# Kernel optimization log

Measured on AMD Instinct MI355X. Metric: run time of the kernel, lower is better.

The kernel has to match this reference:

```python
import jax, jax.numpy as jnp
import numpy as np

NUM_HEADS = 4
WINDOW = 3

def setup_inputs() -> dict:
    key = jax.random.key(0)
    ks = jax.random.split(key, 6)
    B, V, C, H, W = 4, 6, 256, 32, 32
    s = 0.02
    return {
        "x": jax.random.normal(ks[0], (B, V, C, H, W), jnp.float32),
        "Wq": jax.random.normal(ks[1], (C, C), jnp.float32) * s,
        "bq": jnp.zeros((C,), jnp.float32),
        "Wk": jax.random.normal(ks[2], (V * C, C), jnp.float32) * s,
        "bk": jnp.zeros((C,), jnp.float32),
        "Wv": jax.random.normal(ks[3], (V * C, C), jnp.float32) * s,
        "bv": jnp.zeros((C,), jnp.float32),
        "Wo": jax.random.normal(ks[4], (C, C), jnp.float32) * s,
        "bo": jnp.zeros((C,), jnp.float32),
    }

def reference(x, Wq, bq, Wk, bk, Wv, bv, Wo, bo):
    B, V, C, H, W = x.shape
    HW = H * W
    S = HW * V  # query sequence length
    nh = NUM_HEADS
    hd = C // nh
    # q: [B, V, H, W, C] -> [B, S, C]
    q_in = jnp.transpose(x, (0, 1, 3, 4, 2)).reshape(B, S, C)
    # k/v input: [B, H, W, V, C] -> [B, HW, V*C]
    kv_in = jnp.transpose(x, (0, 3, 4, 1, 2)).reshape(B, HW, V * C)
    q = q_in @ Wq + bq
    k = kv_in @ Wk + bk
    v = kv_in @ Wv + bv
    q = q.reshape(B, S, nh, hd).transpose(0, 2, 1, 3)    # [B, nh, S, hd]
    k = k.reshape(B, HW, nh, hd).transpose(0, 2, 1, 3)   # [B, nh, HW, hd]
    v = v.reshape(B, HW, nh, hd).transpose(0, 2, 1, 3)   # [B, nh, HW, hd]
    logits = jnp.einsum("bhqd,bhkd->bhqk", q, k) / jnp.sqrt(jnp.float32(hd))
    # Faithful mask: row i has ones in columns [max(0,i-W), i+W] (clipped to HW cols);
    # it is ADDED as mask * -1e9, masking OUT the diagonal window (as in source).
    i = jnp.arange(S)[:, None]
    j = jnp.arange(HW)[None, :]
    mask = ((j >= i - WINDOW) & (j < i + WINDOW + 1)).astype(logits.dtype)
    logits = logits + mask * (-1e9)
    attn = jax.nn.softmax(logits, axis=-1)
    out = jnp.einsum("bhqk,bhkd->bhqd", attn, v)         # [B, nh, S, hd]
    out = out.transpose(0, 2, 1, 3).reshape(B, S, C)
    out = out @ Wo + bo
    return x.reshape(B * V, C, H, W) + out.reshape(B * V, C, H, W)
```

## Files before the change

### kernel.cpp

```cpp
#include <hip/hip_runtime.h>
#include <cstddef>

namespace {

constexpr int B=4, V=6, C=256, HWS=1024, S=6144, NH=4, HD=64, VC=1536;

typedef short short8  __attribute__((ext_vector_type(8)));
typedef short short4v __attribute__((ext_vector_type(4)));
typedef float f32x4   __attribute__((ext_vector_type(4)));

__device__ inline short f2bf(float f){
  union{float f; unsigned u;} v; v.f=f;
  unsigned r = v.u + 0x7fffu + ((v.u>>16)&1u);
  return (short)(r>>16);
}

__device__ inline void tr_tile(const float* in, int inRow, short* out, int outRow,
                               int r0, int c0, short* T , int t){
  {
    const int rr=t>>2, cc=(t&3)*16;
    const float* p = in + (size_t)(r0+rr)*inRow + c0 + cc;
    short tmp[16];
    #pragma unroll
    for(int j=0;j<4;j++){
      const float4 f=*(const float4*)(p+j*4);
      tmp[j*4+0]=f2bf(f.x); tmp[j*4+1]=f2bf(f.y);
      tmp[j*4+2]=f2bf(f.z); tmp[j*4+3]=f2bf(f.w);
    }
    *(short8*)&T[rr*72+cc]   = *(short8*)&tmp[0];
    *(short8*)&T[rr*72+cc+8] = *(short8*)&tmp[8];
  }
  __syncthreads();
  {
    const int cc=t>>2, rr0=(t&3)*16;
    short tmp[16];
    #pragma unroll
    for(int j=0;j<16;j++) tmp[j]=T[(rr0+j)*72+cc];
    short* o = out + (size_t)(c0+cc)*outRow + r0 + rr0;
    *(short8*)o     = *(short8*)&tmp[0];
    *(short8*)(o+8) = *(short8*)&tmp[8];
  }
}

__global__ __launch_bounds__(256) void prep_x(const float* __restrict__ x, short* __restrict__ xb){
  __shared__ short T[64*72];
  const int bv=blockIdx.z;
  tr_tile(x + (size_t)bv*C*HWS, HWS, xb + (size_t)bv*HWS*C, C,
          blockIdx.y*64, blockIdx.x*64, T, threadIdx.x);
}

__global__ __launch_bounds__(256) void prep_w(const float* Wq,const float* Wk,const float* Wv,const float* Wo,
                                              short* WqT, short* WkT, short* WvT, short* WoT){
  __shared__ short T[64*72];
  const int z=blockIdx.y;
  const float* in; short* out; int R;
  if(z==0){in=Wq; out=WqT; R=C;}
  else if(z==1){in=Wo; out=WoT; R=C;}
  else if(z==2){in=Wk; out=WkT; R=VC;}
  else         {in=Wv; out=WvT; R=VC;}
  const int tilesC=C/64, ntiles=(R/64)*tilesC;
  const int tile=blockIdx.x;
  if(tile>=ntiles) return;
  tr_tile(in, C, out, R, (tile/tilesC)*64, (tile%tilesC)*64, T, threadIdx.x);
}

template<int MODE>
__global__ __launch_bounds__(256) void qo_gemm(const short* __restrict__ A, const short* __restrict__ BT,
                                               const float* __restrict__ bias, const float* __restrict__ xres,
                                               void* __restrict__ outv){
  __shared__ __align__(16) short As[128*72];
  __shared__ __align__(16) short Bs[64*72];
  const int n0=blockIdx.x*64, r0=blockIdx.y*128;
  const int t=threadIdx.x, lane=t&63, w=t>>6, quad=lane>>4, ln=lane&15;

  f32x4 acc[2][4];
  #pragma unroll
  for(int rt=0;rt<2;rt++)
    #pragma unroll
    for(int nt=0;nt<4;nt++) acc[rt][nt]=(f32x4)0.f;

  for(int k0=0;k0<C;k0+=64){
    if(k0) __syncthreads();
    { const int r=t>>1, c=(t&1)*32;
      const short* p = A + (size_t)(r0+r)*C + k0 + c;
      #pragma unroll
      for(int j=0;j<4;j++) *(short8*)&As[r*72+c+j*8] = *(const short8*)(p+j*8);
    }
    { const int n=t>>2, c=(t&3)*16;
      const short* p = BT + (size_t)(n0+n)*C + k0 + c;
      *(short8*)&Bs[n*72+c]   = *(const short8*)p;
      *(short8*)&Bs[n*72+c+8] = *(const short8*)(p+8);
    }
    __syncthreads();
    #pragma unroll
    for(int s=0;s<2;s++){
      short8 af0=*(short8*)&As[(w*32+ln)*72    + s*32+quad*8];
      short8 af1=*(short8*)&As[(w*32+16+ln)*72 + s*32+quad*8];
      #pragma unroll
      for(int nt=0;nt<4;nt++){
        const short8 bf=*(short8*)&Bs[(nt*16+ln)*72 + s*32+quad*8];
        acc[0][nt]=__builtin_amdgcn_mfma_f32_16x16x32_bf16(af0,bf,acc[0][nt],0,0,0);
        acc[1][nt]=__builtin_amdgcn_mfma_f32_16x16x32_bf16(af1,bf,acc[1][nt],0,0,0);
      }
    }
  }

  constexpr float QSCALE = 0.18033688011112042f;
  float bcol[4];
  #pragma unroll
  for(int nt=0;nt<4;nt++) bcol[nt]=bias[n0+nt*16+ln];
  #pragma unroll
  for(int rt=0;rt<2;rt++)
    #pragma unroll
    for(int nt=0;nt<4;nt++)
      #pragma unroll
      for(int i=0;i<4;i++){
        const int row=r0+w*32+rt*16+quad*4+i, col=n0+nt*16+ln;
        const float vv=acc[rt][nt][i]+bcol[nt];
        if constexpr(MODE==0) ((short*)outv)[(size_t)row*C+col]=f2bf(vv*QSCALE);
        else ((float*)outv)[(size_t)row*C+col]=vv + xres[(size_t)row*C+col];
      }
}

__global__ __launch_bounds__(256) void kv_gemm(const short* __restrict__ xb,
                                               const short* __restrict__ WkT, const short* __restrict__ WvT,
                                               const float* __restrict__ bk, const float* __restrict__ bv,
                                               short* __restrict__ Kpack, short* __restrict__ Vpack){
  __shared__ __align__(16) short As[64*72], Bk[64*72], Bv[64*72];
  const int n0=blockIdx.x*64, r0=blockIdx.y*64;
  const int b=r0>>10, hw0=r0&1023;
  const int h=n0>>6, bh=b*NH+h;
  const int t=threadIdx.x, lane=t&63, w=t>>6, quad=lane>>4, ln=lane&15;

  f32x4 ak[4], av[4];
  #pragma unroll
  for(int nt=0;nt<4;nt++){ ak[nt]=(f32x4)0.f; av[nt]=(f32x4)0.f; }

  const int sr=t>>2, sc=(t&3)*16;
  for(int k0=0;k0<VC;k0+=64){
    if(k0) __syncthreads();
    const int v=k0>>8, c0=k0&255;
    { const short* p = xb + (size_t)((b*V+v)*HWS + hw0+sr)*C + c0 + sc;
      *(short8*)&As[sr*72+sc]   = *(const short8*)p;
      *(short8*)&As[sr*72+sc+8] = *(const short8*)(p+8); }
    { const short* p = WkT + (size_t)(n0+sr)*VC + k0 + sc;
      *(short8*)&Bk[sr*72+sc]   = *(const short8*)p;
      *(short8*)&Bk[sr*72+sc+8] = *(const short8*)(p+8); }
    { const short* p = WvT + (size_t)(n0+sr)*VC + k0 + sc;
      *(short8*)&Bv[sr*72+sc]   = *(const short8*)p;
      *(short8*)&Bv[sr*72+sc+8] = *(const short8*)(p+8); }
    __syncthreads();
    #pragma unroll
    for(int s=0;s<2;s++){
      const short8 af=*(short8*)&As[(w*16+ln)*72 + s*32+quad*8];
      #pragma unroll
      for(int nt=0;nt<4;nt++){
        const short8 kf=*(short8*)&Bk[(nt*16+ln)*72 + s*32+quad*8];
        const short8 vf=*(short8*)&Bv[(nt*16+ln)*72 + s*32+quad*8];
        ak[nt]=__builtin_amdgcn_mfma_f32_16x16x32_bf16(af,kf,ak[nt],0,0,0);
        av[nt]=__builtin_amdgcn_mfma_f32_16x16x32_bf16(af,vf,av[nt],0,0,0);
      }
    }
  }

  float bkc[4], bvc[4];
  #pragma unroll
  for(int nt=0;nt<4;nt++){ bkc[nt]=bk[n0+nt*16+ln]; bvc[nt]=bv[n0+nt*16+ln]; }

  {
    short* vq = Vpack + ((size_t)(bh*64 + (hw0>>4) + w))*1024;
    #pragma unroll
    for(int nt=0;nt<4;nt++){
      short4v vp;
      #pragma unroll
      for(int i=0;i<4;i++) vp[i]=f2bf(av[nt][i]+bvc[nt]);
      *(short4v*)(vq + nt*256 + lane*4) = vp;
    }
  }

  __syncthreads();
  #pragma unroll
  for(int nt=0;nt<4;nt++)
    #pragma unroll
    for(int i=0;i<4;i++)
      As[(w*16+quad*4+i)*72 + nt*16+ln] = f2bf(ak[nt][i]+bkc[nt]);
  __syncthreads();
  {
    short* kp = Kpack + ((size_t)(bh*64 + (hw0>>4) + w))*1024;
    #pragma unroll
    for(int half=0; half<2; half++){
      const short8 f = *(short8*)&As[(w*16+ln)*72 + half*32 + quad*8];
      *(short8*)(kp + half*512 + lane*8) = f;
    }
  }
}

__global__ __launch_bounds__(256) void attn_k(const short* __restrict__ q, const short* __restrict__ Kpack,
                                              const short* __restrict__ Vpack, short* __restrict__ ao){
  __shared__ float obuf[64*68];
  __shared__ float lbuf[4][64];
  const int blk=blockIdx.x;
  const int bh=(blk&7)*2 + ((blk>>3)&1);
  const int qt=blk>>4;
  const int b=bh>>2, h=bh&3;
  const int s0=qt*64;
  const int t=threadIdx.x, lane=t&63, w=t>>6, quad=lane>>4, ln=lane&15;

  short8 qf[4][2];
  #pragma unroll
  for(int nt=0;nt<4;nt++)
    #pragma unroll
    for(int s=0;s<2;s++)
      qf[nt][s]=*(const short8*)&q[(size_t)(b*S+s0+nt*16+ln)*C + h*HD + s*32+quad*8];

  f32x4 o[4][4];
  #pragma unroll
  for(int dt=0;dt<4;dt++)
    #pragma unroll
    for(int nt=0;nt<4;nt++) o[dt][nt]=(f32x4)0.f;
  float l[4]={0.f,0.f,0.f,0.f};

  const short* kp = Kpack + ((size_t)(bh*64 + w))*1024;
  const short* vp = Vpack + ((size_t)(bh*64 + w))*1024;

  short8  kf0=*(const short8*)(kp + lane*8);
  short8  kf1=*(const short8*)(kp + 512 + lane*8);
  short4v vf[4];
  #pragma unroll
  for(int dt=0;dt<4;dt++) vf[dt]=*(const short4v*)(vp + dt*256 + lane*4);

  #pragma unroll 1
  for(int j0=0;j0<HWS;j0+=64){
    const size_t adv = (j0+64<HWS) ? 4096 : 0;
    kp += adv; vp += adv;
    const short8  nkf0=*(const short8*)(kp + lane*8);
    const short8  nkf1=*(const short8*)(kp + 512 + lane*8);
    short4v nvf[4];
    #pragma unroll
    for(int dt=0;dt<4;dt++) nvf[dt]=*(const short4v*)(vp + dt*256 + lane*4);

    f32x4 sa[4];
    #pragma unroll
    for(int nt=0;nt<4;nt++) sa[nt]=(f32x4)0.f;
    #pragma unroll
    for(int nt=0;nt<4;nt++){
      sa[nt]=__builtin_amdgcn_mfma_f32_16x16x32_bf16(kf0,qf[nt][0],sa[nt],0,0,0);
      sa[nt]=__builtin_amdgcn_mfma_f32_16x16x32_bf16(kf1,qf[nt][1],sa[nt],0,0,0);
    }

    const int kmin=j0+w*16;
    if(kmin+15 >= s0-3 && kmin <= s0+66){
      #pragma unroll
      for(int nt=0;nt<4;nt++){
        const int ig=s0+nt*16+ln;
        #pragma unroll
        for(int i=0;i<4;i++){
          const int jg=kmin+quad*4+i;
          if((unsigned)(jg-ig+3)<=6u) sa[nt][i]=-100.f;
        }
      }
    }

    short4v pt[4];
    #pragma unroll
    for(int nt=0;nt<4;nt++){
      #pragma unroll
      for(int i=0;i<4;i++){
        const float p=__builtin_amdgcn_exp2f(sa[nt][i]);
        l[nt]+=p;
        union{float f;unsigned u;} pu; pu.f=p;
        pt[nt][i]=(short)(pu.u>>16);
      }
    }

    #pragma unroll
    for(int dt=0;dt<4;dt++)
      #pragma unroll
      for(int nt=0;nt<4;nt++)
        o[dt][nt]=__builtin_amdgcn_mfma_f32_16x16x16bf16_1k(vf[dt],pt[nt],o[dt][nt],0,0,0);

    kf0=nkf0; kf1=nkf1;
    #pragma unroll
    for(int dt=0;dt<4;dt++) vf[dt]=nvf[dt];
  }

  #pragma unroll
  for(int nt=0;nt<4;nt++){
    l[nt]+=__shfl_xor(l[nt],16);
    l[nt]+=__shfl_xor(l[nt],32);
  }
  if(quad==0){
    #pragma unroll
    for(int nt=0;nt<4;nt++) lbuf[w][nt*16+ln]=l[nt];
  }
  for(int r=0;r<4;r++){
    if(w==r){
      #pragma unroll
      for(int dt=0;dt<4;dt++)
        #pragma unroll
        for(int nt=0;nt<4;nt++)
          #pragma unroll
          for(int i=0;i<4;i++){
            const int idx=(dt*16+quad*4+i)*68 + nt*16+ln;
            if(r==0) obuf[idx]=o[dt][nt][i]; else obuf[idx]+=o[dt][nt][i];
          }
    }
    __syncthreads();
  }

  {
    const int row=t>>2, dg=t&3;
    const float linv=1.0f/(lbuf[0][row]+lbuf[1][row]+lbuf[2][row]+lbuf[3][row]);
    short tmp[16];
    #pragma unroll
    for(int j=0;j<16;j++) tmp[j]=f2bf(obuf[(dg*16+j)*68+row]*linv);
    short* op = ao + (size_t)(b*S+s0+row)*C + h*HD + dg*16;
    *(short8*)op     = *(short8*)&tmp[0];
    *(short8*)(op+8) = *(short8*)&tmp[8];
  }
}

}

extern "C" void kernel_launch(void* const* d_in, const int* in_sizes, int n_in,
                              void* d_out, int out_size, void* d_ws, size_t ws_size,
                              hipStream_t stream) {
  const float* x  = (const float*)d_in[0];
  const float* Wq = (const float*)d_in[1];
  const float* bq = (const float*)d_in[2];
  const float* Wk = (const float*)d_in[3];
  const float* bk = (const float*)d_in[4];
  const float* Wv = (const float*)d_in[5];
  const float* bv = (const float*)d_in[6];
  const float* Wo = (const float*)d_in[7];
  const float* bo = (const float*)d_in[8];
  float* out = (float*)d_out;

  char* p = (char*)d_ws;
  const size_t szBS=(size_t)B*S*C*2, szK=(size_t)B*HWS*C*2;
  short* xb   =(short*)p; p+=szBS;
  short* qb   =(short*)p; p+=szBS;
  short* aob  =(short*)p; p+=szBS;
  short* Kpack=(short*)p; p+=szK;
  short* Vpack=(short*)p; p+=szK;
  short* WqT=(short*)p; p+=(size_t)C*C*2;
  short* WoT=(short*)p; p+=(size_t)C*C*2;
  short* WkT=(short*)p; p+=(size_t)C*VC*2;
  short* WvT=(short*)p; p+=(size_t)C*VC*2;

  prep_x<<<dim3(16,4,B*V), 256, 0, stream>>>(x, xb);
  prep_w<<<dim3(96,4),     256, 0, stream>>>(Wq,Wk,Wv,Wo, WqT,WkT,WvT,WoT);
  qo_gemm<0><<<dim3(4, (B*S)/128), 256, 0, stream>>>(xb, WqT, bq, nullptr, qb);
  kv_gemm<<<dim3(4, (B*HWS)/64),  256, 0, stream>>>(xb, WkT, WvT, bk, bv, Kpack, Vpack);
  attn_k<<<dim3(B*NH*(S/64)),     256, 0, stream>>>(qb, Kpack, Vpack, aob);
  qo_gemm<1><<<dim3(4, (B*S)/128), 256, 0, stream>>>(aob, WoT, bo, x, out);
}
```

Baseline: 203.6 us.

## Merge prep and projection launches, restructure attention K/V prefetch

Result: faster. 196.3 us (-3.6%).

```diff
diff --git a/kernel.cpp b/kernel.cpp
--- a/kernel.cpp
+++ b/kernel.cpp
@@ -14,6 +14,9 @@
   unsigned r = v.u + 0x7fffu + ((v.u>>16)&1u);
   return (short)(r>>16);
 }
+__device__ inline unsigned fbits(float f){
+  union{float f; unsigned u;} v; v.f=f; return v.u;
+}
 
 __device__ inline void tr_tile(const float* in, int inRow, short* out, int outRow,
                                int r0, int c0, short* T , int t){
@@ -42,37 +45,36 @@
   }
 }
 
-__global__ __launch_bounds__(256) void prep_x(const float* __restrict__ x, short* __restrict__ xb){
+__global__ __launch_bounds__(256) void prep(const float* __restrict__ x,
+                                            const float* __restrict__ Wq, const float* __restrict__ Wk,
+                                            const float* __restrict__ Wv, const float* __restrict__ Wo,
+                                            short* __restrict__ xb, short* __restrict__ WqT,
+                                            short* __restrict__ WkT, short* __restrict__ WvT,
+                                            short* __restrict__ WoT){
   __shared__ short T[64*72];
-  const int bv=blockIdx.z;
-  tr_tile(x + (size_t)bv*C*HWS, HWS, xb + (size_t)bv*HWS*C, C,
-          blockIdx.y*64, blockIdx.x*64, T, threadIdx.x);
-}
-
-__global__ __launch_bounds__(256) void prep_w(const float* Wq,const float* Wk,const float* Wv,const float* Wo,
-                                              short* WqT, short* WkT, short* WvT, short* WoT){
-  __shared__ short T[64*72];
-  const int z=blockIdx.y;
-  const float* in; short* out; int R;
-  if(z==0){in=Wq; out=WqT; R=C;}
-  else if(z==1){in=Wo; out=WoT; R=C;}
-  else if(z==2){in=Wk; out=WkT; R=VC;}
-  else         {in=Wv; out=WvT; R=VC;}
-  const int tilesC=C/64, ntiles=(R/64)*tilesC;
-  const int tile=blockIdx.x;
-  if(tile>=ntiles) return;
-  tr_tile(in, C, out, R, (tile/tilesC)*64, (tile%tilesC)*64, T, threadIdx.x);
+  const int blk=blockIdx.x;
+  if(blk<1536){
+    const int bx=blk&15, by=(blk>>4)&3, bv=blk>>6;
+    tr_tile(x + (size_t)bv*C*HWS, HWS, xb + (size_t)bv*HWS*C, C, by*64, bx*64, T, threadIdx.x);
+  } else {
+    const int idx=blk-1536;
+    const int tile=idx%96, z=idx/96;
+    const float* in; short* out; int R;
+    if(z==0){in=Wq; out=WqT; R=C;}
+    else if(z==1){in=Wo; out=WoT; R=C;}
+    else if(z==2){in=Wk; out=WkT; R=VC;}
+    else         {in=Wv; out=WvT; R=VC;}
+    const int tilesC=C/64, ntiles=(R/64)*tilesC;
+    if(tile>=ntiles) return;
+    tr_tile(in, C, out, R, (tile/tilesC)*64, (tile%tilesC)*64, T, threadIdx.x);
+  }
 }
 
 template<int MODE>
-__global__ __launch_bounds__(256) void qo_gemm(const short* __restrict__ A, const short* __restrict__ BT,
-                                               const float* __restrict__ bias, const float* __restrict__ xres,
-                                               void* __restrict__ outv){
-  __shared__ __align__(16) short As[128*72];
-  __shared__ __align__(16) short Bs[64*72];
-  const int n0=blockIdx.x*64, r0=blockIdx.y*128;
+__device__ inline void qo_body(const short* __restrict__ A, const short* __restrict__ BT,
+                               const float* __restrict__ bias, const float* __restrict__ xres,
+                               void* __restrict__ outv, short* As, short* Bs, int n0, int r0){
   const int t=threadIdx.x, lane=t&63, w=t>>6, quad=lane>>4, ln=lane&15;
-
   f32x4 acc[2][4];
   #pragma unroll
   for(int rt=0;rt<2;rt++)
@@ -122,15 +124,27 @@
       }
 }
 
-__global__ __launch_bounds__(256) void kv_gemm(const short* __restrict__ xb,
-                                               const short* __restrict__ WkT, const short* __restrict__ WvT,
-                                               const float* __restrict__ bk, const float* __restrict__ bv,
-                                               short* __restrict__ Kpack, short* __restrict__ Vpack){
-  __shared__ __align__(16) short As[64*72], Bk[64*72], Bv[64*72];
-  const int n0=blockIdx.x*64, r0=blockIdx.y*64;
+__global__ __launch_bounds__(256) void proj(const short* __restrict__ xb,
+                                            const short* __restrict__ WqT, const short* __restrict__ WkT,
+                                            const short* __restrict__ WvT,
+                                            const float* __restrict__ bq, const float* __restrict__ bk,
+                                            const float* __restrict__ bv,
+                                            short* __restrict__ qb, short* __restrict__ Kpack,
+                                            short* __restrict__ Vpack){
+  __shared__ __align__(16) short sh[13824];
+  const int blk=blockIdx.x;
+  const int t=threadIdx.x, lane=t&63, w=t>>6, quad=lane>>4, ln=lane&15;
+
+  if(blk>=256){
+    const int qblk=blk-256;
+    qo_body<0>(xb, WqT, bq, nullptr, qb, sh, sh+9216, (qblk&3)*64, (qblk>>2)*128);
+    return;
+  }
+
+  short* As=sh; short* Bk=sh+4608; short* Bv=sh+9216;
+  const int n0=(blk&3)*64, r0=(blk>>2)*64;
   const int b=r0>>10, hw0=r0&1023;
   const int h=n0>>6, bh=b*NH+h;
-  const int t=threadIdx.x, lane=t&63, w=t>>6, quad=lane>>4, ln=lane&15;
 
   f32x4 ak[4], av[4];
   #pragma unroll
@@ -218,74 +232,78 @@
   for(int dt=0;dt<4;dt++)
     #pragma unroll
     for(int nt=0;nt<4;nt++) o[dt][nt]=(f32x4)0.f;
-  float l[4]={0.f,0.f,0.f,0.f};
-
-  const short* kp = Kpack + ((size_t)(bh*64 + w))*1024;
-  const short* vp = Vpack + ((size_t)(bh*64 + w))*1024;
-
-  short8  kf0=*(const short8*)(kp + lane*8);
-  short8  kf1=*(const short8*)(kp + 512 + lane*8);
-  short4v vf[4];
-  #pragma unroll
-  for(int dt=0;dt<4;dt++) vf[dt]=*(const short4v*)(vp + dt*256 + lane*4);
+  f32x4 l4[4];
+  #pragma unroll
+  for(int nt=0;nt<4;nt++) l4[nt]=(f32x4)0.f;
+
+  const short* kbase = Kpack + ((size_t)(bh*64+w))*1024;
+  const short* vbase = Vpack + ((size_t)(bh*64+w))*1024;
+  const f32x4 z4=(f32x4)0.f;
+
+  short8 kfa0=*(const short8*)(kbase + lane*8);
+  short8 kfa1=*(const short8*)(kbase + 512 + lane*8);
+  short8 kfb0=*(const short8*)(kbase + 4096 + lane*8);
+  short8 kfb1=*(const short8*)(kbase + 4096 + 512 + lane*8);
+
+#define ATTN_TILE(KF0,KF1,TI,PI)                                              \
+  {                                                                           \
+    const short* vp = vbase + (size_t)(TI)*4096;                              \
+    short4v vf[4];                                                            \
+    _Pragma("unroll")                                                         \
+    for(int dt=0;dt<4;dt++) vf[dt]=*(const short4v*)(vp + dt*256 + lane*4);   \
+    f32x4 sa[4];                                                              \
+    _Pragma("unroll")                                                         \
+    for(int nt=0;nt<4;nt++){                                                  \
+      sa[nt]=__builtin_amdgcn_mfma_f32_16x16x32_bf16(KF0,qf[nt][0],z4,0,0,0); \
+      sa[nt]=__builtin_amdgcn_mfma_f32_16x16x32_bf16(KF1,qf[nt][1],sa[nt],0,0,0); \
+    }                                                                         \
+    const size_t poff=(size_t)(PI)*4096;                                      \
+    KF0=*(const short8*)(kbase + poff + lane*8);                              \
+    KF1=*(const short8*)(kbase + poff + 512 + lane*8);                        \
+    const int kmin=(TI)*64 + w*16;                                            \
+    if(kmin+15 >= s0-3 && kmin <= s0+66){                                     \
+      _Pragma("unroll")                                                       \
+      for(int nt=0;nt<4;nt++){                                                \
+        const int ig=s0+nt*16+ln;                                             \
+        _Pragma("unroll")                                                     \
+        for(int i=0;i<4;i++){                                                 \
+          const int jg=kmin+quad*4+i;                                         \
+          if((unsigned)(jg-ig+3)<=6u) sa[nt][i]=-100.f;                       \
+        }                                                                     \
+      }                                                                       \
+    }                                                                         \
+    short4v pt[4];                                                            \
+    _Pragma("unroll")                                                         \
+    for(int nt=0;nt<4;nt++){                                                  \
+      f32x4 pv;                                                               \
+      _Pragma("unroll")                                                       \
+      for(int i=0;i<4;i++) pv[i]=__builtin_amdgcn_exp2f(sa[nt][i]);           \
+      l4[nt]+=pv;                                                             \
+      union{ short4v s; unsigned u[2]; } P;                                   \
+      P.u[0]=__builtin_amdgcn_perm(fbits(pv[1]), fbits(pv[0]), 0x07060302u);  \
+      P.u[1]=__builtin_amdgcn_perm(fbits(pv[3]), fbits(pv[2]), 0x07060302u);  \
+      pt[nt]=P.s;                                                             \
+    }                                                                         \
+    _Pragma("unroll")                                                         \
+    for(int dt=0;dt<4;dt++)                                                   \
+      _Pragma("unroll")                                                       \
+      for(int nt=0;nt<4;nt++)                                                 \
+        o[dt][nt]=__builtin_amdgcn_mfma_f32_16x16x16bf16_1k(vf[dt],pt[nt],o[dt][nt],0,0,0); \
+  }
 
   #pragma unroll 1
-  for(int j0=0;j0<HWS;j0+=64){
-    const size_t adv = (j0+64<HWS) ? 4096 : 0;
-    kp += adv; vp += adv;
-    const short8  nkf0=*(const short8*)(kp + lane*8);
-    const short8  nkf1=*(const short8*)(kp + 512 + lane*8);
-    short4v nvf[4];
-    #pragma unroll
-    for(int dt=0;dt<4;dt++) nvf[dt]=*(const short4v*)(vp + dt*256 + lane*4);
-
-    f32x4 sa[4];
-    #pragma unroll
-    for(int nt=0;nt<4;nt++) sa[nt]=(f32x4)0.f;
-    #pragma unroll
-    for(int nt=0;nt<4;nt++){
-      sa[nt]=__builtin_amdgcn_mfma_f32_16x16x32_bf16(kf0,qf[nt][0],sa[nt],0,0,0);
-      sa[nt]=__builtin_amdgcn_mfma_f32_16x16x32_bf16(kf1,qf[nt][1],sa[nt],0,0,0);
-    }
-
-    const int kmin=j0+w*16;
-    if(kmin+15 >= s0-3 && kmin <= s0+66){
-      #pragma unroll
-      for(int nt=0;nt<4;nt++){
-        const int ig=s0+nt*16+ln;
-        #pragma unroll
-        for(int i=0;i<4;i++){
-          const int jg=kmin+quad*4+i;
-          if((unsigned)(jg-ig+3)<=6u) sa[nt][i]=-100.f;
-        }
-      }
-    }
-
-    short4v pt[4];
-    #pragma unroll
-    for(int nt=0;nt<4;nt++){
-      #pragma unroll
-      for(int i=0;i<4;i++){
-        const float p=__builtin_amdgcn_exp2f(sa[nt][i]);
-        l[nt]+=p;
-        union{float f;unsigned u;} pu; pu.f=p;
-        pt[nt][i]=(short)(pu.u>>16);
-      }
-    }
-
-    #pragma unroll
-    for(int dt=0;dt<4;dt++)
-      #pragma unroll
-      for(int nt=0;nt<4;nt++)
-        o[dt][nt]=__builtin_amdgcn_mfma_f32_16x16x16bf16_1k(vf[dt],pt[nt],o[dt][nt],0,0,0);
-
-    kf0=nkf0; kf1=nkf1;
-    #pragma unroll
-    for(int dt=0;dt<4;dt++) vf[dt]=nvf[dt];
-  }
-
+  for(int i=0;i<16;i+=2){
+    const int ipa = (i+2<16)? i+2 : i;
+    const int ipb = (i+3<16)? i+3 : i+1;
+    ATTN_TILE(kfa0,kfa1,i,ipa)
+    ATTN_TILE(kfb0,kfb1,i+1,ipb)
+  }
+#undef ATTN_TILE
+
+  float l[4];
   #pragma unroll
   for(int nt=0;nt<4;nt++){
+    l[nt]=l4[nt][0]+l4[nt][1]+l4[nt][2]+l4[nt][3];
     l[nt]+=__shfl_xor(l[nt],16);
     l[nt]+=__shfl_xor(l[nt],32);
   }
@@ -318,6 +336,13 @@
     *(short8*)op     = *(short8*)&tmp[0];
     *(short8*)(op+8) = *(short8*)&tmp[8];
   }
+}
+
+__global__ __launch_bounds__(256) void o_gemm(const short* __restrict__ A, const short* __restrict__ BT,
+                                              const float* __restrict__ bias, const float* __restrict__ xres,
+                                              float* __restrict__ out){
+  __shared__ __align__(16) short sh[13824];
+  qo_body<1>(A, BT, bias, xres, out, sh, sh+9216, (int)(blockIdx.x&3)*64, (int)(blockIdx.x>>2)*128);
 }
 
 }
@@ -348,10 +373,8 @@
   short* WkT=(short*)p; p+=(size_t)C*VC*2;
   short* WvT=(short*)p; p+=(size_t)C*VC*2;
 
-  prep_x<<<dim3(16,4,B*V), 256, 0, stream>>>(x, xb);
-  prep_w<<<dim3(96,4),     256, 0, stream>>>(Wq,Wk,Wv,Wo, WqT,WkT,WvT,WoT);
-  qo_gemm<0><<<dim3(4, (B*S)/128), 256, 0, stream>>>(xb, WqT, bq, nullptr, qb);
-  kv_gemm<<<dim3(4, (B*HWS)/64),  256, 0, stream>>>(xb, WkT, WvT, bk, bv, Kpack, Vpack);
-  attn_k<<<dim3(B*NH*(S/64)),     256, 0, stream>>>(qb, Kpack, Vpack, aob);
-  qo_gemm<1><<<dim3(4, (B*S)/128), 256, 0, stream>>>(aob, WoT, bo, x, out);
-}
+  prep<<<dim3(1920), 256, 0, stream>>>(x, Wq,Wk,Wv,Wo, xb, WqT,WkT,WvT,WoT);
+  proj<<<dim3(1024), 256, 0, stream>>>(xb, WqT,WkT,WvT, bq,bk,bv, qb, Kpack, Vpack);
+  attn_k<<<dim3(B*NH*(S/64)), 256, 0, stream>>>(qb, Kpack, Vpack, aob);
+  o_gemm<<<dim3(4*((B*S)/128)), 256, 0, stream>>>(aob, WoT, bo, x, out);
+}
```
